# Optimization experiments

Measured on AMD Instinct MI355X. Metric: run time of the kernel, lower is better.

Reference implementation:

```python
import jax, jax.numpy as jnp
import numpy as np

EPS = 1e-5

def _binarize(x):
    # torch.sign with 0 -> +1 (module maps sign==0 to 1)
    return jnp.where(x >= 0, 1.0, -1.0).astype(x.dtype)

def _conv(x, w, stride):
    return jax.lax.conv_general_dilated(
        x, w, window_strides=(stride, stride), padding=((1, 1), (1, 1)),
        dimension_numbers=('NCHW', 'OIHW', 'NCHW'))

def _bn(x, g, b, m, v):
    # eval-mode BatchNorm2d with running stats
    inv = g / jnp.sqrt(v + EPS)
    return x * inv[None, :, None, None] + (b - m * inv)[None, :, None, None]

def setup_inputs() -> dict:
    key = jax.random.key(0)
    ks = jax.random.split(key, 16)
    d = {
        'x': jax.random.normal(ks[0], (32, 3, 224, 224), jnp.float32),
        'conv1_w': jax.random.normal(ks[1], (32, 3, 3, 3), jnp.float32),
        'conv2_w': jax.random.normal(ks[2], (64, 32, 3, 3), jnp.float32),
        'conv3_w': jax.random.normal(ks[3], (128, 64, 3, 3), jnp.float32),
        'bn1_g': jax.random.normal(ks[4], (32,), jnp.float32),
        'bn1_b': jax.random.normal(ks[5], (32,), jnp.float32),
        'bn1_m': jax.random.normal(ks[6], (32,), jnp.float32),
        'bn1_v': jax.random.uniform(ks[7], (32,), jnp.float32, 0.5, 1.5),
        'bn2_g': jax.random.normal(ks[8], (64,), jnp.float32),
        'bn2_b': jax.random.normal(ks[9], (64,), jnp.float32),
        'bn2_m': jax.random.normal(ks[10], (64,), jnp.float32),
        'bn2_v': jax.random.uniform(ks[11], (64,), jnp.float32, 0.5, 1.5),
        'bn3_g': jax.random.normal(ks[12], (128,), jnp.float32),
        'bn3_b': jax.random.normal(ks[13], (128,), jnp.float32),
        'bn3_m': jax.random.normal(ks[14], (128,), jnp.float32),
        'bn3_v': jax.random.uniform(ks[15], (128,), jnp.float32, 0.5, 1.5),
        'fc_w': jax.random.normal(jax.random.fold_in(key, 99), (2, 128), jnp.float32) * 0.1,
        'fc_b': jnp.zeros((2,), jnp.float32),
    }
    return d

def reference(x, conv1_w, conv2_w, conv3_w,
              bn1_g, bn1_b, bn1_m, bn1_v,
              bn2_g, bn2_b, bn2_m, bn2_v,
              bn3_g, bn3_b, bn3_m, bn3_v,
              fc_w, fc_b):
    # layer 1: binarized conv -> BN -> sign
    h = _binarize(_bn(_conv(_binarize(x), _binarize(conv1_w), 1), bn1_g, bn1_b, bn1_m, bn1_v))  # [B,32,224,224]
    # layer 2 (stride 2)
    h = _binarize(_bn(_conv(_binarize(h), _binarize(conv2_w), 2), bn2_g, bn2_b, bn2_m, bn2_v))  # [B,64,112,112]
    # layer 3 (stride 2)
    h = _binarize(_bn(_conv(_binarize(h), _binarize(conv3_w), 2), bn3_g, bn3_b, bn3_m, bn3_v))  # [B,128,56,56]
    # adaptive avg pool to 1x1 + fc
    h = jnp.mean(h, axis=(2, 3))  # [B,128]
    return h @ fc_w.T + fc_b      # [B,2]
```

## Files before the change

### kernel.cpp

```cpp
#include <hip/hip_runtime.h>
#include <cstdint>
#include <cstddef>


__device__ uint32_t g_h1p[32 * 224 * 224];
__device__ uint32_t g_h2lo[32 * 112 * 112];
__device__ uint32_t g_h2hi[32 * 112 * 112];
__device__ uint32_t g_w1p[32];
__device__ uint32_t g_w2p[576];
__device__ uint64_t g_w3p[1152];
__device__ float    g_inv1[32],  g_sh1[32];
__device__ float    g_inv2[64],  g_sh2[64];
__device__ float    g_inv3[128], g_sh3[128];
__device__ int      g_acc[32 * 128];

__global__ void prep_kernel(
    const float* __restrict__ w1, const float* __restrict__ w2, const float* __restrict__ w3,
    const float* __restrict__ g1, const float* __restrict__ b1, const float* __restrict__ m1, const float* __restrict__ v1,
    const float* __restrict__ g2, const float* __restrict__ b2, const float* __restrict__ m2, const float* __restrict__ v2,
    const float* __restrict__ g3, const float* __restrict__ b3, const float* __restrict__ m3, const float* __restrict__ v3)
{
    int tid = blockIdx.x * blockDim.x + threadIdx.x;

    if (tid < 32 * 128) g_acc[tid] = 0;

    if (tid < 32) {
        uint32_t m = 0;
        for (int t = 0; t < 27; ++t)
            m |= (w1[tid * 27 + t] < 0.0f ? 1u : 0u) << t;
        g_w1p[tid] = m;
    }
    if (tid < 576) {
        int oc = tid / 9, tap = tid % 9, ky = tap / 3, kx = tap % 3;
        uint32_t m = 0;
        for (int ic = 0; ic < 32; ++ic)
            m |= (w2[((oc * 32 + ic) * 3 + ky) * 3 + kx] < 0.0f ? 1u : 0u) << ic;
        g_w2p[tid] = m;
    }
    if (tid < 1152) {
        int oc = tid / 9, tap = tid % 9, ky = tap / 3, kx = tap % 3;
        uint64_t m = 0;
        for (int ic = 0; ic < 64; ++ic)
            m |= (uint64_t)(w3[((oc * 64 + ic) * 3 + ky) * 3 + kx] < 0.0f ? 1u : 0u) << ic;
        g_w3p[tid] = m;
    }
    if (tid < 32) {
        float inv = __fdiv_rn(g1[tid], __fsqrt_rn(__fadd_rn(v1[tid], 1e-5f)));
        g_inv1[tid] = inv;
        g_sh1[tid] = __fsub_rn(b1[tid], __fmul_rn(m1[tid], inv));
    } else if (tid < 96) {
        int c = tid - 32;
        float inv = __fdiv_rn(g2[c], __fsqrt_rn(__fadd_rn(v2[c], 1e-5f)));
        g_inv2[c] = inv;
        g_sh2[c] = __fsub_rn(b2[c], __fmul_rn(m2[c], inv));
    } else if (tid < 224) {
        int c = tid - 96;
        float inv = __fdiv_rn(g3[c], __fsqrt_rn(__fadd_rn(v3[c], 1e-5f)));
        g_inv3[c] = inv;
        g_sh3[c] = __fsub_rn(b3[c], __fmul_rn(m3[c], inv));
    }
}

__global__ void layer1_kernel(const float* __restrict__ x)
{
    int idx = blockIdx.x * blockDim.x + threadIdx.x;
    const int total = 32 * 224 * 224;
    if (idx >= total) return;
    int xx = idx % 224;
    int t = idx / 224;
    int yy = t % 224;
    int b = t / 224;

    const float* xb = x + (size_t)b * 3 * 224 * 224;
    uint32_t xmask = 0, vmask = 0;
#pragma unroll
    for (int ky = 0; ky < 3; ++ky) {
        int iy = yy - 1 + ky;
        bool vy = (iy >= 0 && iy < 224);
#pragma unroll
        for (int kx = 0; kx < 3; ++kx) {
            int ix = xx - 1 + kx;
            bool v = vy && (ix >= 0) && (ix < 224);
            if (v) {
                int sp = ky * 3 + kx;
#pragma unroll
                for (int ic = 0; ic < 3; ++ic) {
                    float val = xb[(ic * 224 + iy) * 224 + ix];
                    xmask |= (val < 0.0f ? 1u : 0u) << (ic * 9 + sp);
                    vmask |= 1u << (ic * 9 + sp);
                }
            }
        }
    }
    int nvalid = __popc(vmask);
    uint32_t outw = 0;
#pragma unroll
    for (int oc = 0; oc < 32; ++oc) {
        int mism = __popc((xmask ^ g_w1p[oc]) & vmask);
        int s = nvalid - 2 * mism;
        float y = __fadd_rn(__fmul_rn((float)s, g_inv1[oc]), g_sh1[oc]);
        outw |= (y < 0.0f ? 1u : 0u) << oc;
    }
    g_h1p[idx] = outw;
}

__global__ void layer2_kernel()
{
    int half = blockIdx.y;

    int idx = blockIdx.x * blockDim.x + threadIdx.x;
    const int total = 32 * 112 * 112;
    if (idx >= total) return;
    int ox = idx % 112;
    int t = idx / 112;
    int oy = t % 112;
    int b = t / 112;

    const uint32_t* hb = g_h1p + (size_t)b * 224 * 224;
    uint32_t hw[9];
    bool tv[9];
    int nvt = 0;
#pragma unroll
    for (int ky = 0; ky < 3; ++ky) {
        int iy = 2 * oy - 1 + ky;
        bool vy = (iy >= 0 && iy < 224);
#pragma unroll
        for (int kx = 0; kx < 3; ++kx) {
            int ix = 2 * ox - 1 + kx;
            bool v = vy && (ix >= 0) && (ix < 224);
            int tt = ky * 3 + kx;
            tv[tt] = v;
            nvt += v ? 1 : 0;
            hw[tt] = v ? hb[iy * 224 + ix] : 0u;
        }
    }
#pragma unroll
    for (int tt = 0; tt < 9; ++tt)
        if (!tv[tt]) hw[tt] = 0u;

    int base = 32 * nvt;
    const uint32_t* wp = g_w2p + half * 32 * 9;
    const float* invp = g_inv2 + half * 32;
    const float* shp  = g_sh2  + half * 32;
    uint32_t outw = 0;
    for (int oc = 0; oc < 32; ++oc) {
        int s = 0;
#pragma unroll
        for (int tt = 0; tt < 9; ++tt) {
            uint32_t w = wp[oc * 9 + tt];
            s += __popc(hw[tt] ^ (tv[tt] ? w : 0u));
        }
        int val = base - 2 * s;
        float y = __fadd_rn(__fmul_rn((float)val, invp[oc]), shp[oc]);
        outw |= (y < 0.0f ? 1u : 0u) << oc;
    }
    if (half == 0) g_h2lo[idx] = outw; else g_h2hi[idx] = outw;
}

__global__ void layer3_kernel()
{
    int ocq = blockIdx.z;

    int b = blockIdx.y;
    int pix = blockIdx.x * blockDim.x + threadIdx.x;
    bool valid = pix < 56 * 56;
    int oy = valid ? pix / 56 : 0;
    int ox = valid ? pix % 56 : 0;

    const uint32_t* hlo = g_h2lo + (size_t)b * 112 * 112;
    const uint32_t* hhi = g_h2hi + (size_t)b * 112 * 112;
    uint64_t hw[9];
    bool tv[9];
    int nvt = 0;
#pragma unroll
    for (int ky = 0; ky < 3; ++ky) {
        int iy = 2 * oy - 1 + ky;
        bool vy = (iy >= 0 && iy < 112);
#pragma unroll
        for (int kx = 0; kx < 3; ++kx) {
            int ix = 2 * ox - 1 + kx;
            bool v = valid && vy && (ix >= 0) && (ix < 112);
            int tt = ky * 3 + kx;
            tv[tt] = v;
            nvt += v ? 1 : 0;
            hw[tt] = v ? ((uint64_t)hlo[iy * 112 + ix] | ((uint64_t)hhi[iy * 112 + ix] << 32)) : 0ull;
        }
    }
    int base = 64 * nvt;
    int lane = threadIdx.x & 63;
    unsigned long long am = __ballot(valid ? 1 : 0);
    int nact = __popcll(am);

    const uint64_t* wp = g_w3p + ocq * 32 * 9;
    const float* invp = g_inv3 + ocq * 32;
    const float* shp  = g_sh3  + ocq * 32;
    for (int oc = 0; oc < 32; ++oc) {
        int s = 0;
#pragma unroll
        for (int tt = 0; tt < 9; ++tt) {
            uint64_t w = wp[oc * 9 + tt];
            s += __popcll(hw[tt] ^ (tv[tt] ? w : 0ull));
        }
        int val = base - 2 * s;
        float y = __fadd_rn(__fmul_rn((float)val, invp[oc]), shp[oc]);
        int neg = (valid && y < 0.0f) ? 1 : 0;
        unsigned long long bm = __ballot(neg);
        if (lane == 0) {
            int cneg = __popcll(bm);
            atomicAdd(&g_acc[b * 128 + ocq * 32 + oc], nact - 2 * cneg);
        }
    }
}

__global__ void fc_kernel(
    const float* __restrict__ fc_w, const float* __restrict__ fc_b,
    float* __restrict__ out)
{
    int tid = threadIdx.x;
    if (tid >= 64) return;
    int b = tid >> 1, k = tid & 1;
    float s = fc_b[k];
    for (int oc = 0; oc < 128; ++oc) {
        float h = __fdiv_rn((float)g_acc[b * 128 + oc], 3136.0f);
        s = __fadd_rn(s, __fmul_rn(h, fc_w[k * 128 + oc]));
    }
    out[b * 2 + k] = s;
}

extern "C" void kernel_launch(void* const* d_in, const int* in_sizes, int n_in,
                              void* d_out, int out_size, void* d_ws, size_t ws_size,
                              hipStream_t stream)
{
    const float* x   = (const float*)d_in[0];
    const float* w1  = (const float*)d_in[1];
    const float* w2  = (const float*)d_in[2];
    const float* w3  = (const float*)d_in[3];
    const float* g1  = (const float*)d_in[4];
    const float* b1  = (const float*)d_in[5];
    const float* m1  = (const float*)d_in[6];
    const float* v1  = (const float*)d_in[7];
    const float* g2  = (const float*)d_in[8];
    const float* b2  = (const float*)d_in[9];
    const float* m2  = (const float*)d_in[10];
    const float* v2  = (const float*)d_in[11];
    const float* g3  = (const float*)d_in[12];
    const float* b3  = (const float*)d_in[13];
    const float* m3  = (const float*)d_in[14];
    const float* v3  = (const float*)d_in[15];
    const float* fcw = (const float*)d_in[16];
    const float* fcb = (const float*)d_in[17];
    float* out = (float*)d_out;
    (void)d_ws; (void)ws_size; (void)in_sizes; (void)n_in; (void)out_size;

    prep_kernel<<<16, 256, 0, stream>>>(w1, w2, w3,
        g1, b1, m1, v1, g2, b2, m2, v2, g3, b3, m3, v3);

    {
        int total = 32 * 224 * 224;
        layer1_kernel<<<(total + 255) / 256, 256, 0, stream>>>(x);
    }
    {
        int total = 32 * 112 * 112;
        dim3 grid((total + 255) / 256, 2);
        layer2_kernel<<<grid, 256, 0, stream>>>();
    }
    {
        dim3 grid((56 * 56 + 255) / 256, 32, 4);
        layer3_kernel<<<grid, 256, 0, stream>>>();
    }
    fc_kernel<<<1, 64, 0, stream>>>(fcw, fcb, out);
}
```

Baseline: 197.4 us.

## Precompute BN sign thresholds, vectorize layer1 four pixels per thread, fuse FC into layer3

Replaces the per-channel float BN+sign in layers 1 and 2 with integer mismatch-count thresholds and a polarity mask, precomputed once in the prep kernel. Layer1 now computes four adjacent pixels per thread with row bitmasks and a 16-byte store, and interior pixels skip bounds checks. Layer3 switches to 64-thread blocks that divide the pixel count exactly and runs the FC in the last-arriving block, which removes one launch. The threshold search is exact for monotone BN, but the threshold equivalence relies on the integer and float comparisons matching at the boundary.

```diff
diff --git a/kernel.cpp b/kernel.cpp
--- a/kernel.cpp
+++ b/kernel.cpp
@@ -3,16 +3,26 @@
 #include <cstddef>
 
 
-__device__ uint32_t g_h1p[32 * 224 * 224];
-__device__ uint32_t g_h2lo[32 * 112 * 112];
-__device__ uint32_t g_h2hi[32 * 112 * 112];
+__device__ __align__(16) uint32_t g_h1p[32 * 224 * 224];
+__device__ __align__(16) uint32_t g_h2lo[32 * 112 * 112];
+__device__ __align__(16) uint32_t g_h2hi[32 * 112 * 112];
 __device__ uint32_t g_w1p[32];
 __device__ uint32_t g_w2p[576];
 __device__ uint64_t g_w3p[1152];
 __device__ float    g_inv1[32],  g_sh1[32];
 __device__ float    g_inv2[64],  g_sh2[64];
 __device__ float    g_inv3[128], g_sh3[128];
+__device__ int      g_thr1[32];
+__device__ uint32_t g_pol1;
+__device__ int      g_thr2[64];
+__device__ uint32_t g_pol2[2];
 __device__ int      g_acc[32 * 128];
+__device__ int      g_done;
+
+__device__ __forceinline__ int bn_neg(int s, float inv, float sh) {
+    float y = __fadd_rn(__fmul_rn((float)s, inv), sh);
+    return (y < 0.0f) ? 1 : 0;
+}
 
 __global__ void prep_kernel(
     const float* __restrict__ w1, const float* __restrict__ w2, const float* __restrict__ w3,
@@ -21,8 +31,10 @@
     const float* __restrict__ g3, const float* __restrict__ b3, const float* __restrict__ m3, const float* __restrict__ v3)
 {
     int tid = blockIdx.x * blockDim.x + threadIdx.x;
+    int lt  = threadIdx.x;
 
     if (tid < 32 * 128) g_acc[tid] = 0;
+    if (tid == 0) g_done = 0;
 
     if (tid < 32) {
         uint32_t m = 0;
@@ -44,70 +56,155 @@
             m |= (uint64_t)(w3[((oc * 64 + ic) * 3 + ky) * 3 + kx] < 0.0f ? 1u : 0u) << ic;
         g_w3p[tid] = m;
     }
-    if (tid < 32) {
-        float inv = __fdiv_rn(g1[tid], __fsqrt_rn(__fadd_rn(v1[tid], 1e-5f)));
-        g_inv1[tid] = inv;
-        g_sh1[tid] = __fsub_rn(b1[tid], __fmul_rn(m1[tid], inv));
-    } else if (tid < 96) {
-        int c = tid - 32;
-        float inv = __fdiv_rn(g2[c], __fsqrt_rn(__fadd_rn(v2[c], 1e-5f)));
-        g_inv2[c] = inv;
-        g_sh2[c] = __fsub_rn(b2[c], __fmul_rn(m2[c], inv));
-    } else if (tid < 224) {
-        int c = tid - 96;
-        float inv = __fdiv_rn(g3[c], __fsqrt_rn(__fadd_rn(v3[c], 1e-5f)));
-        g_inv3[c] = inv;
-        g_sh3[c] = __fsub_rn(b3[c], __fmul_rn(m3[c], inv));
+
+    if (blockIdx.x == 0) {
+        if (lt < 32) {
+            float inv = __fdiv_rn(g1[lt], __fsqrt_rn(__fadd_rn(v1[lt], 1e-5f)));
+            g_inv1[lt] = inv;
+            g_sh1[lt] = __fsub_rn(b1[lt], __fmul_rn(m1[lt], inv));
+        } else if (lt < 96) {
+            int c = lt - 32;
+            float inv = __fdiv_rn(g2[c], __fsqrt_rn(__fadd_rn(v2[c], 1e-5f)));
+            g_inv2[c] = inv;
+            g_sh2[c] = __fsub_rn(b2[c], __fmul_rn(m2[c], inv));
+        } else if (lt < 224) {
+            int c = lt - 96;
+            float inv = __fdiv_rn(g3[c], __fsqrt_rn(__fadd_rn(v3[c], 1e-5f)));
+            g_inv3[c] = inv;
+            g_sh3[c] = __fsub_rn(b3[c], __fmul_rn(m3[c], inv));
+        }
+        __syncthreads();
+
+        __shared__ uint32_t p1bits[32];
+        __shared__ uint32_t p2bits[64];
+        if (lt < 32) {
+            float inv = g_inv1[lt], sh = g_sh1[lt];
+            int P = bn_neg(27 - 2 * 27, inv, sh);
+            int M = 28;
+            for (int m = 0; m <= 27; ++m)
+                if (bn_neg(27 - 2 * m, inv, sh) == P) { M = m; break; }
+            g_thr1[lt] = M;
+            p1bits[lt] = (uint32_t)P;
+        }
+        if (lt >= 64 && lt < 128) {
+            int c = lt - 64;
+            float inv = g_inv2[c], sh = g_sh2[c];
+            int P = bn_neg(288 - 2 * 288, inv, sh);
+            int M = 289;
+            for (int m = 0; m <= 288; ++m)
+                if (bn_neg(288 - 2 * m, inv, sh) == P) { M = m; break; }
+            g_thr2[c] = M;
+            p2bits[c] = (uint32_t)P;
+        }
+        __syncthreads();
+        if (lt == 0) {
+            uint32_t p = 0;
+            for (int i = 0; i < 32; ++i) p |= p1bits[i] << i;
+            g_pol1 = p;
+            uint32_t plo = 0, phi = 0;
+            for (int i = 0; i < 32; ++i) { plo |= p2bits[i] << i; phi |= p2bits[32 + i] << i; }
+            g_pol2[0] = plo; g_pol2[1] = phi;
+        }
     }
 }
 
 __global__ void layer1_kernel(const float* __restrict__ x)
 {
     int idx = blockIdx.x * blockDim.x + threadIdx.x;
-    const int total = 32 * 224 * 224;
+    const int total = 32 * 224 * 56;
     if (idx >= total) return;
-    int xx = idx % 224;
-    int t = idx / 224;
+    int xq = idx % 56;
+    int t  = idx / 56;
     int yy = t % 224;
-    int b = t / 224;
+    int b  = t / 224;
+    int xx0 = xq * 4;
 
     const float* xb = x + (size_t)b * 3 * 224 * 224;
-    uint32_t xmask = 0, vmask = 0;
-#pragma unroll
-    for (int ky = 0; ky < 3; ++ky) {
-        int iy = yy - 1 + ky;
-        bool vy = (iy >= 0 && iy < 224);
-#pragma unroll
-        for (int kx = 0; kx < 3; ++kx) {
-            int ix = xx - 1 + kx;
-            bool v = vy && (ix >= 0) && (ix < 224);
-            if (v) {
-                int sp = ky * 3 + kx;
-#pragma unroll
-                for (int ic = 0; ic < 3; ++ic) {
-                    float val = xb[(ic * 224 + iy) * 224 + ix];
-                    xmask |= (val < 0.0f ? 1u : 0u) << (ic * 9 + sp);
-                    vmask |= 1u << (ic * 9 + sp);
+    uint32_t outw[4];
+
+    bool interior = (yy >= 1) && (yy <= 222) && (xq >= 1) && (xq <= 54);
+    if (interior) {
+        uint32_t cb[3][3];
+#pragma unroll
+        for (int ic = 0; ic < 3; ++ic)
+#pragma unroll
+        for (int r = 0; r < 3; ++r) {
+            const float* p = xb + ((size_t)ic * 224 + (yy - 1 + r)) * 224 + (xx0 - 1);
+            uint32_t bits = 0;
+#pragma unroll
+            for (int j = 0; j < 6; ++j)
+                bits |= (p[j] < 0.0f ? 1u : 0u) << j;
+            cb[ic][r] = bits;
+        }
+        uint32_t xm[4];
+#pragma unroll
+        for (int p = 0; p < 4; ++p) {
+            uint32_t m = 0;
+#pragma unroll
+            for (int ic = 0; ic < 3; ++ic)
+#pragma unroll
+            for (int r = 0; r < 3; ++r)
+                m |= ((cb[ic][r] >> p) & 7u) << (ic * 9 + r * 3);
+            xm[p] = m;
+        }
+#pragma unroll
+        for (int p = 0; p < 4; ++p) outw[p] = 0;
+#pragma unroll
+        for (int oc = 0; oc < 32; ++oc) {
+            uint32_t w = g_w1p[oc];
+            int M = g_thr1[oc];
+#pragma unroll
+            for (int p = 0; p < 4; ++p) {
+                int mm = __popc(xm[p] ^ w);
+                outw[p] |= (mm < M ? 1u : 0u) << oc;
+            }
+        }
+        uint32_t pol = g_pol1;
+#pragma unroll
+        for (int p = 0; p < 4; ++p) outw[p] ^= pol;
+    } else {
+#pragma unroll
+        for (int p = 0; p < 4; ++p) {
+            int xx = xx0 + p;
+            uint32_t xmask = 0, vmask = 0;
+#pragma unroll
+            for (int ky = 0; ky < 3; ++ky) {
+                int iy = yy - 1 + ky;
+                bool vy = (iy >= 0 && iy < 224);
+#pragma unroll
+                for (int kx = 0; kx < 3; ++kx) {
+                    int ix = xx - 1 + kx;
+                    bool v = vy && (ix >= 0) && (ix < 224);
+                    if (v) {
+                        int sp = ky * 3 + kx;
+#pragma unroll
+                        for (int ic = 0; ic < 3; ++ic) {
+                            float val = xb[((size_t)ic * 224 + iy) * 224 + ix];
+                            xmask |= (val < 0.0f ? 1u : 0u) << (ic * 9 + sp);
+                            vmask |= 1u << (ic * 9 + sp);
+                        }
+                    }
                 }
             }
-        }
-    }
-    int nvalid = __popc(vmask);
-    uint32_t outw = 0;
-#pragma unroll
-    for (int oc = 0; oc < 32; ++oc) {
-        int mism = __popc((xmask ^ g_w1p[oc]) & vmask);
-        int s = nvalid - 2 * mism;
-        float y = __fadd_rn(__fmul_rn((float)s, g_inv1[oc]), g_sh1[oc]);
-        outw |= (y < 0.0f ? 1u : 0u) << oc;
-    }
-    g_h1p[idx] = outw;
+            int nvalid = __popc(vmask);
+            uint32_t ow = 0;
+#pragma unroll
+            for (int oc = 0; oc < 32; ++oc) {
+                int mism = __popc((xmask ^ g_w1p[oc]) & vmask);
+                int s = nvalid - 2 * mism;
+                float y = __fadd_rn(__fmul_rn((float)s, g_inv1[oc]), g_sh1[oc]);
+                ow |= (y < 0.0f ? 1u : 0u) << oc;
+            }
+            outw[p] = ow;
+        }
+    }
+    uint4 o = make_uint4(outw[0], outw[1], outw[2], outw[3]);
+    *(uint4*)&g_h1p[((size_t)b * 224 + yy) * 224 + xx0] = o;
 }
 
 __global__ void layer2_kernel()
 {
     int half = blockIdx.y;
-
     int idx = blockIdx.x * blockDim.x + threadIdx.x;
     const int total = 32 * 112 * 112;
     if (idx >= total) return;
@@ -117,55 +214,73 @@
     int b = t / 112;
 
     const uint32_t* hb = g_h1p + (size_t)b * 224 * 224;
-    uint32_t hw[9];
-    bool tv[9];
-    int nvt = 0;
-#pragma unroll
-    for (int ky = 0; ky < 3; ++ky) {
-        int iy = 2 * oy - 1 + ky;
-        bool vy = (iy >= 0 && iy < 224);
-#pragma unroll
-        for (int kx = 0; kx < 3; ++kx) {
-            int ix = 2 * ox - 1 + kx;
-            bool v = vy && (ix >= 0) && (ix < 224);
-            int tt = ky * 3 + kx;
-            tv[tt] = v;
-            nvt += v ? 1 : 0;
-            hw[tt] = v ? hb[iy * 224 + ix] : 0u;
-        }
-    }
-#pragma unroll
-    for (int tt = 0; tt < 9; ++tt)
-        if (!tv[tt]) hw[tt] = 0u;
-
-    int base = 32 * nvt;
-    const uint32_t* wp = g_w2p + half * 32 * 9;
-    const float* invp = g_inv2 + half * 32;
-    const float* shp  = g_sh2  + half * 32;
+    const uint32_t* wp = g_w2p + half * 288;
     uint32_t outw = 0;
-    for (int oc = 0; oc < 32; ++oc) {
-        int s = 0;
-#pragma unroll
-        for (int tt = 0; tt < 9; ++tt) {
-            uint32_t w = wp[oc * 9 + tt];
-            s += __popc(hw[tt] ^ (tv[tt] ? w : 0u));
-        }
-        int val = base - 2 * s;
-        float y = __fadd_rn(__fmul_rn((float)val, invp[oc]), shp[oc]);
-        outw |= (y < 0.0f ? 1u : 0u) << oc;
+
+    if (ox >= 1 && oy >= 1) {
+        uint32_t hw[9];
+#pragma unroll
+        for (int ky = 0; ky < 3; ++ky) {
+            const uint32_t* row = hb + (2 * oy - 1 + ky) * 224 + (2 * ox - 1);
+            hw[ky * 3 + 0] = row[0];
+            hw[ky * 3 + 1] = row[1];
+            hw[ky * 3 + 2] = row[2];
+        }
+        const int* thr = g_thr2 + half * 32;
+        for (int oc = 0; oc < 32; ++oc) {
+            int m = 0;
+#pragma unroll
+            for (int tt = 0; tt < 9; ++tt)
+                m += __popc(hw[tt] ^ wp[oc * 9 + tt]);
+            outw |= (m < thr[oc] ? 1u : 0u) << oc;
+        }
+        outw ^= g_pol2[half];
+    } else {
+        uint32_t hw[9];
+        bool tv[9];
+        int nvt = 0;
+#pragma unroll
+        for (int ky = 0; ky < 3; ++ky) {
+            int iy = 2 * oy - 1 + ky;
+            bool vy = (iy >= 0 && iy < 224);
+#pragma unroll
+            for (int kx = 0; kx < 3; ++kx) {
+                int ix = 2 * ox - 1 + kx;
+                bool v = vy && (ix >= 0) && (ix < 224);
+                int tt = ky * 3 + kx;
+                tv[tt] = v;
+                nvt += v ? 1 : 0;
+                hw[tt] = v ? hb[iy * 224 + ix] : 0u;
+            }
+        }
+        int base = 32 * nvt;
+        const float* invp = g_inv2 + half * 32;
+        const float* shp  = g_sh2  + half * 32;
+        for (int oc = 0; oc < 32; ++oc) {
+            int s = 0;
+#pragma unroll
+            for (int tt = 0; tt < 9; ++tt) {
+                uint32_t w = wp[oc * 9 + tt];
+                s += __popc(hw[tt] ^ (tv[tt] ? w : 0u));
+            }
+            int val = base - 2 * s;
+            float y = __fadd_rn(__fmul_rn((float)val, invp[oc]), shp[oc]);
+            outw |= (y < 0.0f ? 1u : 0u) << oc;
+        }
     }
     if (half == 0) g_h2lo[idx] = outw; else g_h2hi[idx] = outw;
 }
 
-__global__ void layer3_kernel()
+__global__ void layer3_kernel(
+    const float* __restrict__ fcw, const float* __restrict__ fcb,
+    float* __restrict__ out)
 {
     int ocq = blockIdx.z;
-
     int b = blockIdx.y;
-    int pix = blockIdx.x * blockDim.x + threadIdx.x;
-    bool valid = pix < 56 * 56;
-    int oy = valid ? pix / 56 : 0;
-    int ox = valid ? pix % 56 : 0;
+    int lane = threadIdx.x;
+    int pix = blockIdx.x * 64 + lane;
+    int oy = pix / 56;
+    int ox = pix % 56;
 
     const uint32_t* hlo = g_h2lo + (size_t)b * 112 * 112;
     const uint32_t* hhi = g_h2hi + (size_t)b * 112 * 112;
@@ -179,7 +294,7 @@
 #pragma unroll
         for (int kx = 0; kx < 3; ++kx) {
             int ix = 2 * ox - 1 + kx;
-            bool v = valid && vy && (ix >= 0) && (ix < 112);
+            bool v = vy && (ix >= 0) && (ix < 112);
             int tt = ky * 3 + kx;
             tv[tt] = v;
             nvt += v ? 1 : 0;
@@ -187,11 +302,8 @@
         }
     }
     int base = 64 * nvt;
-    int lane = threadIdx.x & 63;
-    unsigned long long am = __ballot(valid ? 1 : 0);
-    int nact = __popcll(am);
-
-    const uint64_t* wp = g_w3p + ocq * 32 * 9;
+
+    const uint64_t* wp = g_w3p + ocq * 288;
     const float* invp = g_inv3 + ocq * 32;
     const float* shp  = g_sh3  + ocq * 32;
     for (int oc = 0; oc < 32; ++oc) {
@@ -203,28 +315,28 @@
         }
         int val = base - 2 * s;
         float y = __fadd_rn(__fmul_rn((float)val, invp[oc]), shp[oc]);
-        int neg = (valid && y < 0.0f) ? 1 : 0;
-        unsigned long long bm = __ballot(neg);
+        unsigned long long bm = __ballot(y < 0.0f ? 1 : 0);
         if (lane == 0) {
             int cneg = __popcll(bm);
-            atomicAdd(&g_acc[b * 128 + ocq * 32 + oc], nact - 2 * cneg);
-        }
-    }
-}
-
-__global__ void fc_kernel(
-    const float* __restrict__ fc_w, const float* __restrict__ fc_b,
-    float* __restrict__ out)
-{
-    int tid = threadIdx.x;
-    if (tid >= 64) return;
-    int b = tid >> 1, k = tid & 1;
-    float s = fc_b[k];
-    for (int oc = 0; oc < 128; ++oc) {
-        float h = __fdiv_rn((float)g_acc[b * 128 + oc], 3136.0f);
-        s = __fadd_rn(s, __fmul_rn(h, fc_w[k * 128 + oc]));
-    }
-    out[b * 2 + k] = s;
+            atomicAdd(&g_acc[b * 128 + ocq * 32 + oc], 64 - 2 * cneg);
+        }
+    }
+
+    __threadfence();
+    int prev = 0;
+    if (lane == 0)
+        prev = __hip_atomic_fetch_add(&g_done, 1, __ATOMIC_ACQ_REL, __HIP_MEMORY_SCOPE_AGENT);
+    prev = __shfl(prev, 0);
+    if (prev == 49 * 32 * 4 - 1) {
+        int bb = lane >> 1, k = lane & 1;
+        float s = fcb[k];
+        for (int oc = 0; oc < 128; ++oc) {
+            int a = __hip_atomic_load(&g_acc[bb * 128 + oc], __ATOMIC_RELAXED, __HIP_MEMORY_SCOPE_AGENT);
+            float h = __fdiv_rn((float)a, 3136.0f);
+            s = __fadd_rn(s, __fmul_rn(h, fcw[k * 128 + oc]));
+        }
+        out[bb * 2 + k] = s;
+    }
 }
 
 extern "C" void kernel_launch(void* const* d_in, const int* in_sizes, int n_in,
@@ -256,7 +368,7 @@
         g1, b1, m1, v1, g2, b2, m2, v2, g3, b3, m3, v3);
 
     {
-        int total = 32 * 224 * 224;
+        int total = 32 * 224 * 56;
         layer1_kernel<<<(total + 255) / 256, 256, 0, stream>>>(x);
     }
     {
@@ -265,8 +377,7 @@
         layer2_kernel<<<grid, 256, 0, stream>>>();
     }
     {
-        dim3 grid((56 * 56 + 255) / 256, 32, 4);
-        layer3_kernel<<<grid, 256, 0, stream>>>();
-    }
-    fc_kernel<<<1, 64, 0, stream>>>(fcw, fcb, out);
-}
+        dim3 grid(49, 32, 4);
+        layer3_kernel<<<grid, 64, 0, stream>>>(fcw, fcb, out);
+    }
+}
```

Measured after the change: 403.6 us. 104% more time.
